# Optimization experiments

Hardware: AMD Instinct MI355X
Metric: run time of the kernel (lower is better)

Reference implementation:

```python
import jax, jax.numpy as jnp
import numpy as np

N = 100_000      # nodes
E = 3_200_000    # edges (avg degree 32)
F_IN, H, C = 1433, 16, 7


def setup_inputs() -> dict:
    key = jax.random.key(0)
    ks = jax.random.split(key, 8)
    x = jax.random.normal(ks[0], (N, F_IN), jnp.float32)
    edge_index = jax.random.randint(ks[1], (2, E), 0, N, dtype=jnp.int32)
    s_in = 1.0 / np.sqrt(F_IN)
    s_h = 1.0 / np.sqrt(H)
    w_root1 = jax.random.normal(ks[2], (F_IN, H), jnp.float32) * s_in
    w_rel1 = jax.random.normal(ks[3], (F_IN, H), jnp.float32) * s_in
    b_rel1 = jnp.zeros((H,), jnp.float32)
    w_root2 = jax.random.normal(ks[4], (H, C), jnp.float32) * s_h
    w_rel2 = jax.random.normal(ks[5], (H, C), jnp.float32) * s_h
    b_rel2 = jnp.zeros((C,), jnp.float32)
    return {"x": x, "edge_index": edge_index,
            "w_root1": w_root1, "w_rel1": w_rel1, "b_rel1": b_rel1,
            "w_root2": w_root2, "w_rel2": w_rel2, "b_rel2": b_rel2}


def _graph_conv(x, src, dst, w_root, w_rel, b_rel, n_nodes):
    # GraphConv: out_i = W_root x_i + W_rel * sum_{j->i} x_j + b.
    # Sum-aggregation commutes with the linear map, so project first
    # (avoids gathering full-width features per edge).
    h = x @ w_rel                                   # [N, out]
    agg = jax.ops.segment_sum(h[src], dst, num_segments=n_nodes)  # [N, out]
    return agg + b_rel + x @ w_root


def reference(x, edge_index, w_root1, w_rel1, b_rel1, w_root2, w_rel2, b_rel2):
    src, dst = edge_index[0], edge_index[1]
    h1 = jax.nn.elu(_graph_conv(x, src, dst, w_root1, w_rel1, b_rel1, N))
    # F.dropout(training=self.training) -> identity in eval mode
    h2 = _graph_conv(h1, src, dst, w_root2, w_rel2, b_rel2, N)
    return jax.nn.log_softmax(h2, axis=1)
```

## Files before the change

### kernel.cpp

```cpp
#include <hip/hip_runtime.h>
#include <math.h>

#define FIN  1433
#define HID  16
#define NCLS 7
#define BM   128
#define BK   32
#define KS   2
#define KT_TOTAL 45
#define KT_HALF  23

__global__ __launch_bounds__(256) void k1_gemm(
    const float* __restrict__ x,
    const float* __restrict__ w_root, const float* __restrict__ w_rel,
    const float* __restrict__ b_rel,
    float* __restrict__ pa, float* __restrict__ pb,
    float* __restrict__ aa, float* __restrict__ ab, int n) {
  __shared__ float xs[BK * BM];
  __shared__ float ws[BK * 32];

  const int tid   = threadIdx.x;
  const int row0  = blockIdx.x * BM;
  const int slice = blockIdx.y;
  const int cg    = tid & 7;
  const int rg    = tid >> 3;
  const int c0    = cg * 4;
  const int r0    = rg * 4;

  const int kt_beg = slice == 0 ? 0 : KT_HALF;
  const int kt_end = slice == 0 ? KT_HALF : KT_TOTAL;

  float acc[4][4];
#pragma unroll
  for (int i = 0; i < 4; ++i)
#pragma unroll
    for (int j = 0; j < 4; ++j) acc[i][j] = 0.f;

  float xreg[16], wreg[4];

  auto prefetch = [&](int kt) {
    const int k0 = kt * BK;
#pragma unroll
    for (int i = 0; i < 16; ++i) {
      int idx = i * 256 + tid;
      int r = idx >> 5, c = idx & 31;
      int gr = row0 + r, gk = k0 + c;
      xreg[i] = (gr < n && gk < FIN) ? x[(size_t)gr * FIN + gk] : 0.f;
    }
#pragma unroll
    for (int i = 0; i < 4; ++i) {
      int idx = i * 256 + tid;
      int kk = idx >> 5, c = idx & 31;
      int gk = k0 + kk;
      float v = 0.f;
      if (gk < FIN) v = (c < HID) ? w_rel[gk * HID + c] : w_root[gk * HID + (c - HID)];
      wreg[i] = v;
    }
  };

  prefetch(kt_beg);
  for (int kt = kt_beg; kt < kt_end; ++kt) {
    __syncthreads();
#pragma unroll
    for (int i = 0; i < 16; ++i) {
      int idx = i * 256 + tid;
      int r = idx >> 5, c = idx & 31;
      xs[c * BM + (r ^ c)] = xreg[i];
    }
#pragma unroll
    for (int i = 0; i < 4; ++i) {
      int idx = i * 256 + tid;
      int kk = idx >> 5, c = idx & 31;
      ws[kk * 32 + c] = wreg[i];
    }
    __syncthreads();
    if (kt + 1 < kt_end) prefetch(kt + 1);
#pragma unroll
    for (int kk = 0; kk < BK; ++kk) {
      float4 xv = *(const float4*)&xs[kk * BM + ((r0 ^ kk) & ~3)];
      float4 wv = *(const float4*)&ws[kk * 32 + c0];
      float comp[4] = {xv.x, xv.y, xv.z, xv.w};
      const int p = kk & 3;
      float xa[4] = {comp[0 ^ p], comp[1 ^ p], comp[2 ^ p], comp[3 ^ p]};
      float wa[4] = {wv.x, wv.y, wv.z, wv.w};
#pragma unroll
      for (int i = 0; i < 4; ++i)
#pragma unroll
        for (int j = 0; j < 4; ++j)
          acc[i][j] = fmaf(xa[i], wa[j], acc[i][j]);
    }
  }

  float* __restrict__ p_out = slice == 0 ? pa : pb;
  float* __restrict__ a_out = slice == 0 ? aa : ab;
  if (cg < 4) {
#pragma unroll
    for (int i = 0; i < 4; ++i) {
      int gr = row0 + r0 + i;
      if (gr < n) {
        float4 v = {acc[i][0], acc[i][1], acc[i][2], acc[i][3]};
        *(float4*)&p_out[(size_t)gr * HID + c0] = v;
      }
    }
  } else {
    const int cb = c0 - HID;
    float b0 = 0.f, b1 = 0.f, b2v = 0.f, b3 = 0.f;
    if (slice == 0) { b0 = b_rel[cb]; b1 = b_rel[cb+1]; b2v = b_rel[cb+2]; b3 = b_rel[cb+3]; }
#pragma unroll
    for (int i = 0; i < 4; ++i) {
      int gr = row0 + r0 + i;
      if (gr < n) {
        float4 v = {acc[i][0] + b0, acc[i][1] + b1, acc[i][2] + b2v, acc[i][3] + b3};
        *(float4*)&a_out[(size_t)gr * HID + cb] = v;
      }
    }
  }
}

__global__ __launch_bounds__(256) void k_reduce(
    float* __restrict__ pa, const float* __restrict__ pb,
    float* __restrict__ aa, const float* __restrict__ ab, int n4) {
  int i = blockIdx.x * 256 + threadIdx.x;
  if (i >= n4) return;
  float4 a = ((const float4*)pa)[i], b = ((const float4*)pb)[i];
  a.x += b.x; a.y += b.y; a.z += b.z; a.w += b.w;
  ((float4*)pa)[i] = a;
  float4 c = ((const float4*)aa)[i], d = ((const float4*)ab)[i];
  c.x += d.x; c.y += d.y; c.z += d.z; c.w += d.w;
  ((float4*)aa)[i] = c;
}

__global__ __launch_bounds__(256) void k2_scatter16(
    const int* __restrict__ ei, const float* __restrict__ p,
    float* __restrict__ agg, int nE) {
  long long tid = (long long)blockIdx.x * 256 + threadIdx.x;
  if (tid >= (long long)nE * HID) return;
  int e = (int)(tid >> 4), f = (int)(tid & 15);
  int s = ei[e], d = ei[nE + e];
  atomicAdd(agg + (size_t)d * HID + f, p[(size_t)s * HID + f]);
}

__global__ __launch_bounds__(256) void k3_l2(
    const float* __restrict__ agg,
    const float* __restrict__ w_root2, const float* __restrict__ w_rel2,
    const float* __restrict__ b2,
    float* __restrict__ p2, float* __restrict__ out2, int n) {
  int i = blockIdx.x * 256 + threadIdx.x;
  if (i >= n) return;
  const float4* a4 = (const float4*)(agg + (size_t)i * HID);
  float h[HID];
#pragma unroll
  for (int q = 0; q < 4; ++q) {
    float4 v = a4[q];
    float t[4] = {v.x, v.y, v.z, v.w};
#pragma unroll
    for (int j = 0; j < 4; ++j)
      h[4*q + j] = t[j] > 0.f ? t[j] : expm1f(t[j]);
  }
#pragma unroll
  for (int c = 0; c < NCLS; ++c) {
    float sr = 0.f, so = b2[c];
#pragma unroll
    for (int k = 0; k < HID; ++k) {
      sr = fmaf(h[k], w_rel2[k * NCLS + c], sr);
      so = fmaf(h[k], w_root2[k * NCLS + c], so);
    }
    p2[(size_t)i * NCLS + c] = sr;
    out2[(size_t)i * NCLS + c] = so;
  }
}

__global__ __launch_bounds__(256) void k4_scatter7(
    const int* __restrict__ ei, const float* __restrict__ p,
    float* __restrict__ out2, int nE) {
  long long tid = (long long)blockIdx.x * 256 + threadIdx.x;
  int e = (int)(tid >> 3), f = (int)(tid & 7);
  if (e >= nE || f >= NCLS) return;
  int s = ei[e], d = ei[nE + e];
  atomicAdd(out2 + (size_t)d * NCLS + f, p[(size_t)s * NCLS + f]);
}

__global__ __launch_bounds__(256) void k5_lsm(float* __restrict__ out, int n) {
  int i = blockIdx.x * 256 + threadIdx.x;
  if (i >= n) return;
  float v[NCLS];
  float* o = out + (size_t)i * NCLS;
#pragma unroll
  for (int c = 0; c < NCLS; ++c) v[c] = o[c];
  float m = v[0];
#pragma unroll
  for (int c = 1; c < NCLS; ++c) m = fmaxf(m, v[c]);
  float s = 0.f;
#pragma unroll
  for (int c = 0; c < NCLS; ++c) s += expf(v[c] - m);
  float l = logf(s);
#pragma unroll
  for (int c = 0; c < NCLS; ++c) o[c] = v[c] - m - l;
}

extern "C" void kernel_launch(void* const* d_in, const int* in_sizes, int n_in,
                              void* d_out, int out_size, void* d_ws, size_t ws_size,
                              hipStream_t stream) {
  const float* x       = (const float*)d_in[0];
  const int*   ei      = (const int*)  d_in[1];
  const float* w_root1 = (const float*)d_in[2];
  const float* w_rel1  = (const float*)d_in[3];
  const float* b_rel1  = (const float*)d_in[4];
  const float* w_root2 = (const float*)d_in[5];
  const float* w_rel2  = (const float*)d_in[6];
  const float* b_rel2  = (const float*)d_in[7];
  float* out = (float*)d_out;

  int n  = in_sizes[0] / FIN;
  int nE = in_sizes[1] / 2;

  size_t seg = (size_t)n * HID * 4;
  char* ws = (char*)d_ws;
  float* pa = (float*)(ws + 0 * seg);
  float* pb = (float*)(ws + 1 * seg);
  float* aa = (float*)(ws + 2 * seg);
  float* ab = (float*)(ws + 3 * seg);
  float* p2 = (float*)(ws + 4 * seg);

  dim3 g1((n + BM - 1) / BM, KS);
  k1_gemm<<<g1, 256, 0, stream>>>(x, w_root1, w_rel1, b_rel1, pa, pb, aa, ab, n);

  int n4 = n * HID / 4;
  k_reduce<<<(n4 + 255) / 256, 256, 0, stream>>>(pa, pb, aa, ab, n4);

  long long t2 = (long long)nE * HID;
  k2_scatter16<<<(int)((t2 + 255) / 256), 256, 0, stream>>>(ei, pa, aa, nE);

  int nb = (n + 255) / 256;
  k3_l2<<<nb, 256, 0, stream>>>(aa, w_root2, w_rel2, b_rel2, p2, out, n);

  long long t4 = (long long)nE * 8;
  k4_scatter7<<<(int)((t4 + 255) / 256), 256, 0, stream>>>(ei, p2, out, nE);

  k5_lsm<<<nb, 256, 0, stream>>>(out, n);
}
```

Measured before the change: 599.1 us.

## Build CSR by destination each call and replace atomic scatters with gathers

Each call now builds a destination-sorted CSR from the edge list (histogram, single-block scan, atomic placement). Both graph aggregations then become per-node gather-sums with no float atomics, where before they were per-edge atomic scatters. The first GEMM's K dimension is also split four ways instead of two, which raises block count at the cost of more partial buffers to reduce. The CSR build costs two atomic passes over the edges plus a serial single-block scan over 100k nodes, and the gathers can be load-imbalanced across nodes.

Result: slower. 973.2 us (+62.5%).

```diff
diff --git a/kernel.cpp b/kernel.cpp
--- a/kernel.cpp
+++ b/kernel.cpp
@@ -6,16 +6,15 @@
 #define NCLS 7
 #define BM   128
 #define BK   32
-#define KS   2
+#define KS   4
 #define KT_TOTAL 45
-#define KT_HALF  23
 
 __global__ __launch_bounds__(256) void k1_gemm(
     const float* __restrict__ x,
     const float* __restrict__ w_root, const float* __restrict__ w_rel,
     const float* __restrict__ b_rel,
-    float* __restrict__ pa, float* __restrict__ pb,
-    float* __restrict__ aa, float* __restrict__ ab, int n) {
+    float* __restrict__ pbase, float* __restrict__ abase,
+    size_t seg_elems, int n) {
   __shared__ float xs[BK * BM];
   __shared__ float ws[BK * 32];
 
@@ -27,8 +26,8 @@
   const int c0    = cg * 4;
   const int r0    = rg * 4;
 
-  const int kt_beg = slice == 0 ? 0 : KT_HALF;
-  const int kt_end = slice == 0 ? KT_HALF : KT_TOTAL;
+  const int kt_beg = (KT_TOTAL * slice) / KS;
+  const int kt_end = (KT_TOTAL * (slice + 1)) / KS;
 
   float acc[4][4];
 #pragma unroll
@@ -37,7 +36,6 @@
     for (int j = 0; j < 4; ++j) acc[i][j] = 0.f;
 
   float xreg[16], wreg[4];
-
   auto prefetch = [&](int kt) {
     const int k0 = kt * BK;
 #pragma unroll
@@ -91,8 +89,8 @@
     }
   }
 
-  float* __restrict__ p_out = slice == 0 ? pa : pb;
-  float* __restrict__ a_out = slice == 0 ? aa : ab;
+  float* __restrict__ p_out = pbase + (size_t)slice * seg_elems;
+  float* __restrict__ a_out = abase + (size_t)slice * seg_elems;
   if (cg < 4) {
 #pragma unroll
     for (int i = 0; i < 4; ++i) {
@@ -118,26 +116,100 @@
 }
 
 __global__ __launch_bounds__(256) void k_reduce(
-    float* __restrict__ pa, const float* __restrict__ pb,
-    float* __restrict__ aa, const float* __restrict__ ab, int n4) {
+    float* __restrict__ pbase, float* __restrict__ abase,
+    size_t seg_elems, int n4) {
   int i = blockIdx.x * 256 + threadIdx.x;
   if (i >= n4) return;
-  float4 a = ((const float4*)pa)[i], b = ((const float4*)pb)[i];
-  a.x += b.x; a.y += b.y; a.z += b.z; a.w += b.w;
-  ((float4*)pa)[i] = a;
-  float4 c = ((const float4*)aa)[i], d = ((const float4*)ab)[i];
-  c.x += d.x; c.y += d.y; c.z += d.z; c.w += d.w;
-  ((float4*)aa)[i] = c;
-}
-
-__global__ __launch_bounds__(256) void k2_scatter16(
-    const int* __restrict__ ei, const float* __restrict__ p,
-    float* __restrict__ agg, int nE) {
-  long long tid = (long long)blockIdx.x * 256 + threadIdx.x;
-  if (tid >= (long long)nE * HID) return;
-  int e = (int)(tid >> 4), f = (int)(tid & 15);
-  int s = ei[e], d = ei[nE + e];
-  atomicAdd(agg + (size_t)d * HID + f, p[(size_t)s * HID + f]);
+  size_t s4 = seg_elems / 4;
+  float4 a = ((const float4*)pbase)[i];
+  float4 c = ((const float4*)abase)[i];
+#pragma unroll
+  for (int s = 1; s < KS; ++s) {
+    float4 b = ((const float4*)pbase)[i + s * s4];
+    float4 d = ((const float4*)abase)[i + s * s4];
+    a.x += b.x; a.y += b.y; a.z += b.z; a.w += b.w;
+    c.x += d.x; c.y += d.y; c.z += d.z; c.w += d.w;
+  }
+  ((float4*)pbase)[i] = a;
+  ((float4*)abase)[i] = c;
+}
+
+__global__ __launch_bounds__(256) void k_zero(int* __restrict__ p, int n) {
+  int i = blockIdx.x * 256 + threadIdx.x;
+  if (i < n) p[i] = 0;
+}
+
+__global__ __launch_bounds__(256) void k_hist(
+    const int* __restrict__ ei, int* __restrict__ hist, int nE) {
+  int e = blockIdx.x * 256 + threadIdx.x;
+  if (e >= nE) return;
+  atomicAdd(hist + ei[nE + e], 1);
+}
+
+__global__ __launch_bounds__(1024) void k_scan(
+    const int* __restrict__ hist, int* __restrict__ offs,
+    int* __restrict__ cur, int n) {
+  __shared__ int sums[1024];
+  const int tid = threadIdx.x;
+  const int per = (n + 1023) / 1024;
+  const int beg = tid * per;
+  const int end = min(beg + per, n);
+  int s = 0;
+  for (int i = beg; i < end; ++i) s += hist[i];
+  sums[tid] = s;
+  __syncthreads();
+  for (int d = 1; d < 1024; d <<= 1) {
+    int add = (tid >= d) ? sums[tid - d] : 0;
+    __syncthreads();
+    sums[tid] += add;
+    __syncthreads();
+  }
+  int offset = sums[tid] - s;
+  for (int i = beg; i < end; ++i) {
+    offs[i] = offset; cur[i] = offset;
+    offset += hist[i];
+  }
+}
+
+__global__ __launch_bounds__(256) void k_place(
+    const int* __restrict__ ei, int* __restrict__ cur,
+    int* __restrict__ sorted_src, int nE) {
+  int e = blockIdx.x * 256 + threadIdx.x;
+  if (e >= nE) return;
+  int pos = atomicAdd(cur + ei[nE + e], 1);
+  sorted_src[pos] = ei[e];
+}
+
+__global__ __launch_bounds__(256) void k_agg16(
+    const int* __restrict__ sorted_src, const int* __restrict__ offs,
+    const int* __restrict__ hist, const float* __restrict__ p1,
+    float* __restrict__ agg, int n) {
+  long long gt = (long long)blockIdx.x * 256 + threadIdx.x;
+  int d = (int)(gt >> 4), f = (int)(gt & 15);
+  if (d >= n) return;
+  int base = offs[d], deg = hist[d];
+  float acc = 0.f;
+  for (int j = 0; j < deg; ++j) {
+    int s = sorted_src[base + j];
+    acc += p1[(size_t)s * HID + f];
+  }
+  agg[(size_t)d * HID + f] += acc;
+}
+
+__global__ __launch_bounds__(256) void k_agg7(
+    const int* __restrict__ sorted_src, const int* __restrict__ offs,
+    const int* __restrict__ hist, const float* __restrict__ p2,
+    float* __restrict__ out, int n) {
+  long long gt = (long long)blockIdx.x * 256 + threadIdx.x;
+  int d = (int)(gt >> 3), f = (int)(gt & 7);
+  if (d >= n || f >= NCLS) return;
+  int base = offs[d], deg = hist[d];
+  float acc = 0.f;
+  for (int j = 0; j < deg; ++j) {
+    int s = sorted_src[base + j];
+    acc += p2[(size_t)s * NCLS + f];
+  }
+  out[(size_t)d * NCLS + f] += acc;
 }
 
 __global__ __launch_bounds__(256) void k3_l2(
@@ -168,16 +240,6 @@
     p2[(size_t)i * NCLS + c] = sr;
     out2[(size_t)i * NCLS + c] = so;
   }
-}
-
-__global__ __launch_bounds__(256) void k4_scatter7(
-    const int* __restrict__ ei, const float* __restrict__ p,
-    float* __restrict__ out2, int nE) {
-  long long tid = (long long)blockIdx.x * 256 + threadIdx.x;
-  int e = (int)(tid >> 3), f = (int)(tid & 7);
-  if (e >= nE || f >= NCLS) return;
-  int s = ei[e], d = ei[nE + e];
-  atomicAdd(out2 + (size_t)d * NCLS + f, p[(size_t)s * NCLS + f]);
 }
 
 __global__ __launch_bounds__(256) void k5_lsm(float* __restrict__ out, int n) {
@@ -214,28 +276,36 @@
   int n  = in_sizes[0] / FIN;
   int nE = in_sizes[1] / 2;
 
-  size_t seg = (size_t)n * HID * 4;
+  size_t seg = (size_t)n * HID;
   char* ws = (char*)d_ws;
-  float* pa = (float*)(ws + 0 * seg);
-  float* pb = (float*)(ws + 1 * seg);
-  float* aa = (float*)(ws + 2 * seg);
-  float* ab = (float*)(ws + 3 * seg);
-  float* p2 = (float*)(ws + 4 * seg);
+  float* pbase = (float*)ws;
+  float* abase = pbase + KS * seg;
+  float* p2    = abase + KS * seg;
+  int*   hist  = (int*)(p2 + (size_t)n * NCLS);
+  int*   offs  = hist + n;
+  int*   cur   = offs + n;
+  int*   ssrc  = cur + n;
+
+  int nbE = (nE + 255) / 256;
+  int nbN = (n + 255) / 256;
+
+  k_zero<<<nbN, 256, 0, stream>>>(hist, n);
+  k_hist<<<nbE, 256, 0, stream>>>(ei, hist, nE);
+  k_scan<<<1, 1024, 0, stream>>>(hist, offs, cur, n);
+  k_place<<<nbE, 256, 0, stream>>>(ei, cur, ssrc, nE);
 
   dim3 g1((n + BM - 1) / BM, KS);
-  k1_gemm<<<g1, 256, 0, stream>>>(x, w_root1, w_rel1, b_rel1, pa, pb, aa, ab, n);
-
+  k1_gemm<<<g1, 256, 0, stream>>>(x, w_root1, w_rel1, b_rel1,
+                                  pbase, abase, seg, n);
   int n4 = n * HID / 4;
-  k_reduce<<<(n4 + 255) / 256, 256, 0, stream>>>(pa, pb, aa, ab, n4);
-
-  long long t2 = (long long)nE * HID;
-  k2_scatter16<<<(int)((t2 + 255) / 256), 256, 0, stream>>>(ei, pa, aa, nE);
-
-  int nb = (n + 255) / 256;
-  k3_l2<<<nb, 256, 0, stream>>>(aa, w_root2, w_rel2, b_rel2, p2, out, n);
-
-  long long t4 = (long long)nE * 8;
-  k4_scatter7<<<(int)((t4 + 255) / 256), 256, 0, stream>>>(ei, p2, out, nE);
-
-  k5_lsm<<<nb, 256, 0, stream>>>(out, n);
-}
+  k_reduce<<<(n4 + 255) / 256, 256, 0, stream>>>(pbase, abase, seg, n4);
+
+  long long t1 = (long long)n * 16;
+  k_agg16<<<(int)((t1 + 255) / 256), 256, 0, stream>>>(ssrc, offs, hist, pbase, abase, n);
+
+  k3_l2<<<nbN, 256, 0, stream>>>(abase, w_root2, w_rel2, b_rel2, p2, out, n);
+  long long t2 = (long long)n * 8;
+  k_agg7<<<(int)((t2 + 255) / 256), 256, 0, stream>>>(ssrc, offs, hist, p2, out, n);
+
+  k5_lsm<<<nbN, 256, 0, stream>>>(out, n);
+}
```
